# Optimization experiments

Hardware: AMD Instinct MI355X
Metric: run time of the kernel (lower is better)

Reference implementation:

```python
import jax, jax.numpy as jnp
import numpy as np


def setup_inputs() -> dict:
    key = jax.random.key(0)
    ks = jax.random.split(key, 4)
    B, S, D, H, E = 2, 2048, 1024, 4096, 8
    scale_in = 1.0 / np.sqrt(D)
    scale_h = 1.0 / np.sqrt(H)
    return {
        "x": jax.random.normal(ks[0], (B, S, D), dtype=jnp.float32),
        "Wr": jax.random.normal(ks[1], (E, D), dtype=jnp.float32) * scale_in,
        "br": jnp.zeros((E,), dtype=jnp.float32),
        "W1": jax.random.normal(ks[2], (E, H, D), dtype=jnp.float32) * scale_in,
        "b1": jnp.zeros((E, H), dtype=jnp.float32),
        "W2": jax.random.normal(ks[3], (E, D, H), dtype=jnp.float32) * scale_h,
        "b2": jnp.zeros((E, D), dtype=jnp.float32),
        "top_k": 2,
    }


def reference(x, Wr, br, W1, b1, W2, b2, top_k):
    B, S, D = x.shape
    E = Wr.shape[0]
    x_flat = x.reshape(-1, D)                                   # [N, D]
    # Router: top-k logits, softmax over the selected k values only
    logits = x_flat @ Wr.T + br                                 # [N, E]
    top_vals, top_idx = jax.lax.top_k(logits, top_k)            # [N, k]
    gates = jax.nn.softmax(top_vals, axis=-1)                   # [N, k]
    # Per-expert combine weight: gate_e[n, e] = sum_k gates[n, k] * 1[top_idx[n,k]==e]
    gate_e = jnp.einsum("nk,nke->ne", gates,
                        jax.nn.one_hot(top_idx, E, dtype=x.dtype))  # [N, E]
    # Dense all-expert MLP (grouped GEMM), then masked combine. Same math as
    # the per-expert gather/scatter loop: unselected experts get zero gate.
    h = jax.nn.relu(jnp.einsum("nd,ehd->neh", x_flat, W1) + b1)     # [N, E, H]
    y = jnp.einsum("neh,edh->ned", h, W2) + b2                      # [N, E, D]
    out = jnp.einsum("ned,ne->nd", y, gate_e)                       # [N, D]
    return out.reshape(B, S, D)
```

## Files before the change

kernel.cpp:

```cpp
#include <hip/hip_runtime.h>
#include <hip/hip_bf16.h>
#include <stdint.h>

#define N_TOK 4096
#define D_ 1024
#define H_ 4096
#define E_ 8
#define NSLOT (N_TOK*2)
#define BM 128
#define BN 128
#define BK 32
#define MAXT 72

typedef __attribute__((ext_vector_type(8))) short short8;
typedef __attribute__((ext_vector_type(4))) float floatx4;
typedef unsigned int u32;

__device__ __forceinline__ unsigned short f2bf(float f){
    union { float f; unsigned int u; } c; c.f = f;
    unsigned int u = c.u;
    unsigned int r = (u + 0x7fffu + ((u >> 16) & 1u)) >> 16;
    return (unsigned short)r;
}

__device__ __forceinline__ void async16(const void* g, void* l){
    __builtin_amdgcn_global_load_lds(
        (const __attribute__((address_space(1))) u32*)g,
        (__attribute__((address_space(3))) u32*)l, 16, 0, 0);
}


__global__ __launch_bounds__(256) void router_kernel(
    const float* __restrict__ x, const float* __restrict__ Wr,
    const float* __restrict__ br, int* __restrict__ topIdx,
    float* __restrict__ topGate)
{
    int n = blockIdx.x * 4 + (threadIdx.x >> 6);
    int lane = threadIdx.x & 63;
    const float4* xp = (const float4*)(x + (size_t)n * D_);
    float acc[E_];
#pragma unroll
    for (int e = 0; e < E_; e++) acc[e] = 0.f;
#pragma unroll
    for (int j = 0; j < 4; j++){
        int idx = j * 64 + lane;
        float4 xv = xp[idx];
#pragma unroll
        for (int e = 0; e < E_; e++){
            float4 wv = ((const float4*)(Wr + (size_t)e * D_))[idx];
            acc[e] += xv.x*wv.x + xv.y*wv.y + xv.z*wv.z + xv.w*wv.w;
        }
    }
#pragma unroll
    for (int e = 0; e < E_; e++){
        float v = acc[e];
        for (int off = 32; off > 0; off >>= 1) v += __shfl_xor(v, off, 64);
        acc[e] = v;
    }
    if (lane == 0){
        float best = -1e30f, second = -1e30f; int bi = 0, si = 0;
#pragma unroll
        for (int e = 0; e < E_; e++){
            float v = acc[e] + br[e];
            if (v > best){ second = best; si = bi; best = v; bi = e; }
            else if (v > second){ second = v; si = e; }
        }
        float e1 = __expf(second - best);
        float denom = 1.f + e1;
        topIdx[n*2+0] = bi;  topIdx[n*2+1] = si;
        topGate[n*2+0] = 1.f/denom;  topGate[n*2+1] = e1/denom;
    }
}

__global__ __launch_bounds__(256) void hist_kernel(
    const int* __restrict__ topIdx, int* __restrict__ hdr)
{
    __shared__ int c[E_];
    int t = threadIdx.x;
    if (t < E_) c[t] = 0;
    __syncthreads();
    int e = topIdx[blockIdx.x * 256 + t];
    atomicAdd(&c[e], 1);
    __syncthreads();
    if (t < E_) hdr[256 + blockIdx.x * E_ + t] = c[t];
}

__global__ __launch_bounds__(64) void scan2_kernel(int* __restrict__ hdr)
{
    __shared__ int cnt[32 * E_];
    __shared__ int tot[E_];
    __shared__ int offs[E_ + 1];
    int t = threadIdx.x;
    for (int i = t; i < 32 * E_; i += 64) cnt[i] = hdr[256 + i];
    __syncthreads();
    if (t < E_){
        int s = 0;
        for (int b = 0; b < 32; b++) s += cnt[b * E_ + t];
        tot[t] = s;
    }
    __syncthreads();
    if (t == 0){
        int o = 0;
        for (int e = 0; e < E_; e++){ offs[e] = o; o += tot[e]; }
        offs[E_] = o;
    }
    __syncthreads();
    if (t < E_ + 1) hdr[16 + t] = offs[t];
    if (t < E_){
        int run = offs[t];
        for (int b = 0; b < 32; b++){ hdr[512 + b * E_ + t] = run; run += cnt[b * E_ + t]; }
    }
    if (t == 0){
        int tn = 0;
        for (int e = 0; e < E_; e++){
            int nt = (tot[e] + BM - 1) >> 7;
            for (int i = 0; i < nt; i++){ hdr[32 + tn] = e; hdr[112 + tn] = offs[e] + (i << 7); tn++; }
        }
        for (; tn < MAXT; tn++){ hdr[32 + tn] = -1; hdr[112 + tn] = 0; }
    }
}

__global__ __launch_bounds__(256) void pos_kernel(
    const int* __restrict__ topIdx, const float* __restrict__ topGate,
    const int* __restrict__ hdr, int* __restrict__ posOf,
    int* __restrict__ rowTok, float* __restrict__ rowGate)
{
    __shared__ int c[E_];
    int t = threadIdx.x;
    if (t < E_) c[t] = 0;
    __syncthreads();
    int slot = blockIdx.x * 256 + t;
    int e = topIdx[slot];
    int r = atomicAdd(&c[e], 1);
    int pos = hdr[512 + blockIdx.x * E_ + e] + r;
    posOf[slot] = pos;
    rowTok[pos] = slot >> 1;
    rowGate[pos] = topGate[slot];
}

__global__ __launch_bounds__(256) void copy_kernel(
    const float* __restrict__ x, const int* __restrict__ posOf,
    unsigned short* __restrict__ xg)
{
    int slot = blockIdx.x * 4 + (threadIdx.x >> 6);
    int lane = threadIdx.x & 63;
    int n = slot >> 1;
    int pos = posOf[slot];
    const float4* xp = (const float4*)(x + (size_t)n * D_);
    ushort4* op = (ushort4*)(xg + (size_t)pos * D_);
#pragma unroll
    for (int j = 0; j < 4; j++){
        float4 v = xp[j * 64 + lane];
        ushort4 o; o.x=f2bf(v.x); o.y=f2bf(v.y); o.z=f2bf(v.z); o.w=f2bf(v.w);
        op[j * 64 + lane] = o;
    }
}

template<int MODE>
__global__ __launch_bounds__(256) void moe_gemm(
    const unsigned short* __restrict__ A, int Ktot,
    const float* __restrict__ Wbase, size_t wStride,
    const float* __restrict__ biasBase, int biasStride,
    const int* __restrict__ hdr,
    const int* __restrict__ rowTok, const float* __restrict__ rowGate,
    unsigned short* __restrict__ hout, float* __restrict__ out)
{
    const int bx = blockIdx.x, by = blockIdx.y;
    int e = hdr[32 + bx];
    if (e < 0) return;
    int rowBase = hdr[112 + bx];
    int validRows = hdr[16 + e + 1] - rowBase;

    __shared__ __align__(16) unsigned short As[BM * BK];
    __shared__ __align__(16) float Bs[BN * BK];

    const float* Wexp  = Wbase + (size_t)e * wStride + (size_t)(by * BN) * Ktot;
    const float* biasE = biasBase + (size_t)e * biasStride + by * BN;

    const int tid  = threadIdx.x;
    const int lane = tid & 63, wave = tid >> 6;
    const int wm = wave & 1, wn = wave >> 1;
    const int l16 = lane & 15, quad = lane >> 4;

    floatx4 acc[4][4];
#pragma unroll
    for (int mi = 0; mi < 4; mi++)
#pragma unroll
        for (int ni = 0; ni < 4; ni++)
            acc[mi][ni] = (floatx4){0.f,0.f,0.f,0.f};

    int aS[2], aRow[2], aCol[2];
#pragma unroll
    for (int i = 0; i < 2; i++){
        int s = wave * 128 + i * 64 + lane;
        aS[i] = s;
        int r = rowBase + (s >> 2);
        aRow[i] = r < (NSLOT - 1) ? r : (NSLOT - 1);
        aCol[i] = (s & 3) * 8;
    }
    int bS[4], bRow[4], bCol[4];
#pragma unroll
    for (int i = 0; i < 4; i++){
        int s = wave * 256 + i * 64 + lane;
        bS[i] = s;
        int r = s >> 3, c = s & 7;
        bRow[i] = r;
        bCol[i] = (c ^ (r & 7)) * 4;
    }

    for (int k0 = 0; k0 < Ktot; k0 += BK){
#pragma unroll
        for (int i = 0; i < 2; i++)
            async16(A + (size_t)aRow[i] * Ktot + k0 + aCol[i], (char*)As + aS[i] * 16);
#pragma unroll
        for (int i = 0; i < 4; i++)
            async16(Wexp + (size_t)bRow[i] * Ktot + k0 + bCol[i], (char*)Bs + bS[i] * 16);
        __syncthreads();

        short8 af[4];
#pragma unroll
        for (int mi = 0; mi < 4; mi++){
            int r = wm * 64 + mi * 16 + l16;
            af[mi] = *(const short8*)(As + r * BK + quad * 8);
        }
        short8 bfr[4];
#pragma unroll
        for (int ni = 0; ni < 4; ni++){
            int n = wn * 64 + ni * 16 + l16;
            int g0 = (2 * quad)     ^ (n & 7);
            int g1 = (2 * quad + 1) ^ (n & 7);
            float4 u0 = *(const float4*)(Bs + n * BK + g0 * 4);
            float4 u1 = *(const float4*)(Bs + n * BK + g1 * 4);
            union { short8 s; __hip_bfloat162 h[4]; } u;
            u.h[0] = __float22bfloat162_rn(make_float2(u0.x, u0.y));
            u.h[1] = __float22bfloat162_rn(make_float2(u0.z, u0.w));
            u.h[2] = __float22bfloat162_rn(make_float2(u1.x, u1.y));
            u.h[3] = __float22bfloat162_rn(make_float2(u1.z, u1.w));
            bfr[ni] = u.s;
        }
#pragma unroll
        for (int mi = 0; mi < 4; mi++)
#pragma unroll
            for (int ni = 0; ni < 4; ni++)
                acc[mi][ni] = __builtin_amdgcn_mfma_f32_16x16x32_bf16(
                    af[mi], bfr[ni], acc[mi][ni], 0, 0, 0);
        __syncthreads();
    }

#pragma unroll
    for (int mi = 0; mi < 4; mi++){
#pragma unroll
        for (int r = 0; r < 4; r++){
            int rl = wm * 64 + mi * 16 + quad * 4 + r;
            if (rl >= validRows) continue;
            int grow = rowBase + rl;
            int   tok  = 0;
            float gate = 0.f;
            if (MODE == 2){ tok = rowTok[grow]; gate = rowGate[grow]; }
#pragma unroll
            for (int ni = 0; ni < 4; ni++){
                int gcol = by * BN + wn * 64 + ni * 16 + l16;
                float v = acc[mi][ni][r] + biasE[wn * 64 + ni * 16 + l16];
                if (MODE == 1){
                    v = v > 0.f ? v : 0.f;
                    hout[(size_t)grow * H_ + gcol] = f2bf(v);
                } else {
                    atomicAdd(out + (size_t)tok * D_ + gcol, gate * v);
                }
            }
        }
    }
}

extern "C" void kernel_launch(void* const* d_in, const int* in_sizes, int n_in,
                              void* d_out, int out_size, void* d_ws, size_t ws_size,
                              hipStream_t stream)
{
    (void)in_sizes; (void)n_in; (void)ws_size;
    const float* x  = (const float*)d_in[0];
    const float* Wr = (const float*)d_in[1];
    const float* br = (const float*)d_in[2];
    const float* W1 = (const float*)d_in[3];
    const float* b1 = (const float*)d_in[4];
    const float* W2 = (const float*)d_in[5];
    const float* b2 = (const float*)d_in[6];
    float* out = (float*)d_out;

    char* ws = (char*)d_ws;
    int*   hdr     = (int*)ws;
    int*   topIdx  = (int*)  (ws + 4096);
    float* topGate = (float*)(ws + 36864);
    int*   posOf   = (int*)  (ws + 69632);
    int*   rowTok  = (int*)  (ws + 102400);
    float* rowGate = (float*)(ws + 135168);
    unsigned short* xg   = (unsigned short*)(ws + 262144);
    unsigned short* hbuf = (unsigned short*)(ws + 17039360);

    hipMemsetAsync(d_out, 0, (size_t)out_size * sizeof(float), stream);

    router_kernel<<<N_TOK/4, 256, 0, stream>>>(x, Wr, br, topIdx, topGate);
    hist_kernel<<<32, 256, 0, stream>>>(topIdx, hdr);
    scan2_kernel<<<1, 64, 0, stream>>>(hdr);
    pos_kernel<<<32, 256, 0, stream>>>(topIdx, topGate, hdr, posOf, rowTok, rowGate);
    copy_kernel<<<NSLOT/4, 256, 0, stream>>>(x, posOf, xg);
    moe_gemm<1><<<dim3(MAXT, H_/BN), 256, 0, stream>>>(
        xg, D_, W1, (size_t)H_ * D_, b1, H_, hdr, rowTok, rowGate, hbuf, nullptr);
    moe_gemm<2><<<dim3(MAXT, D_/BN), 256, 0, stream>>>(
        hbuf, H_, W2, (size_t)D_ * H_, b2, D_, hdr, rowTok, rowGate, nullptr, out);
}
```

Measured before the change: 649.0 us.

## Pre-convert expert weights to bf16, add split-K for second GEMM and grouped tile order

When the workspace is large enough, W1 and W2 are converted to bf16 in separate passes before the grouped GEMMs. The GEMMs then load bf16 tiles directly, which halves weight traffic and removes the per-tile fp32-to-bf16 conversion. The second GEMM is split along K into two z-slices that accumulate through atomics, with bias added only by slice zero. Block indices are also remapped so groups of eight column tiles run together for better L2 reuse. The conversion passes read 256MB and write 128MB on every call, and the split-K doubles the atomic traffic into the output.

```diff
diff --git a/kernel.cpp b/kernel.cpp
--- a/kernel.cpp
+++ b/kernel.cpp
@@ -29,6 +29,16 @@
         (__attribute__((address_space(3))) u32*)l, 16, 0, 0);
 }
 
+__global__ __launch_bounds__(256) void cvt_kernel(
+    const float* __restrict__ src, unsigned short* __restrict__ dst, int n4)
+{
+    int stride = gridDim.x * 256;
+    for (int i = blockIdx.x * 256 + threadIdx.x; i < n4; i += stride){
+        float4 v = ((const float4*)src)[i];
+        ushort4 o; o.x=f2bf(v.x); o.y=f2bf(v.y); o.z=f2bf(v.z); o.w=f2bf(v.w);
+        ((ushort4*)dst)[i] = o;
+    }
+}
 
 __global__ __launch_bounds__(256) void router_kernel(
     const float* __restrict__ x, const float* __restrict__ Wr,
@@ -156,25 +166,33 @@
     }
 }
 
-template<int MODE>
+template<int MODE, bool BF16B>
 __global__ __launch_bounds__(256) void moe_gemm(
     const unsigned short* __restrict__ A, int Ktot,
-    const float* __restrict__ Wbase, size_t wStride,
+    const void* __restrict__ Wbase, size_t wStride,
     const float* __restrict__ biasBase, int biasStride,
     const int* __restrict__ hdr,
     const int* __restrict__ rowTok, const float* __restrict__ rowGate,
     unsigned short* __restrict__ hout, float* __restrict__ out)
 {
-    const int bx = blockIdx.x, by = blockIdx.y;
+    int gid = blockIdx.y * gridDim.x + blockIdx.x;
+    int per = gridDim.x * 8;
+    int g = gid / per, rr = gid % per;
+    int by = g * 8 + (rr & 7);
+    int bx = rr >> 3;
+
     int e = hdr[32 + bx];
     if (e < 0) return;
     int rowBase = hdr[112 + bx];
     int validRows = hdr[16 + e + 1] - rowBase;
 
+    int kChunk = Ktot / gridDim.z;
+    int kStart = blockIdx.z * kChunk;
+
     __shared__ __align__(16) unsigned short As[BM * BK];
-    __shared__ __align__(16) float Bs[BN * BK];
-
-    const float* Wexp  = Wbase + (size_t)e * wStride + (size_t)(by * BN) * Ktot;
+    __shared__ __align__(16) unsigned short BsH[BF16B ? BN * BK : 1];
+    __shared__ __align__(16) float BsF[BF16B ? 1 : BN * BK];
+
     const float* biasE = biasBase + (size_t)e * biasStride + by * BN;
 
     const int tid  = threadIdx.x;
@@ -192,66 +210,96 @@
     int aS[2], aRow[2], aCol[2];
 #pragma unroll
     for (int i = 0; i < 2; i++){
-        int s = wave * 128 + i * 64 + lane;
+        int s = i * 256 + tid;
         aS[i] = s;
         int r = rowBase + (s >> 2);
         aRow[i] = r < (NSLOT - 1) ? r : (NSLOT - 1);
         aCol[i] = (s & 3) * 8;
     }
-    int bS[4], bRow[4], bCol[4];
-#pragma unroll
-    for (int i = 0; i < 4; i++){
-        int s = wave * 256 + i * 64 + lane;
-        bS[i] = s;
-        int r = s >> 3, c = s & 7;
-        bRow[i] = r;
-        bCol[i] = (c ^ (r & 7)) * 4;
-    }
-
-    for (int k0 = 0; k0 < Ktot; k0 += BK){
-#pragma unroll
-        for (int i = 0; i < 2; i++)
-            async16(A + (size_t)aRow[i] * Ktot + k0 + aCol[i], (char*)As + aS[i] * 16);
-#pragma unroll
-        for (int i = 0; i < 4; i++)
-            async16(Wexp + (size_t)bRow[i] * Ktot + k0 + bCol[i], (char*)Bs + bS[i] * 16);
-        __syncthreads();
-
-        short8 af[4];
-#pragma unroll
-        for (int mi = 0; mi < 4; mi++){
-            int r = wm * 64 + mi * 16 + l16;
-            af[mi] = *(const short8*)(As + r * BK + quad * 8);
-        }
-        short8 bfr[4];
-#pragma unroll
-        for (int ni = 0; ni < 4; ni++){
-            int n = wn * 64 + ni * 16 + l16;
-            int g0 = (2 * quad)     ^ (n & 7);
-            int g1 = (2 * quad + 1) ^ (n & 7);
-            float4 u0 = *(const float4*)(Bs + n * BK + g0 * 4);
-            float4 u1 = *(const float4*)(Bs + n * BK + g1 * 4);
-            union { short8 s; __hip_bfloat162 h[4]; } u;
-            u.h[0] = __float22bfloat162_rn(make_float2(u0.x, u0.y));
-            u.h[1] = __float22bfloat162_rn(make_float2(u0.z, u0.w));
-            u.h[2] = __float22bfloat162_rn(make_float2(u1.x, u1.y));
-            u.h[3] = __float22bfloat162_rn(make_float2(u1.z, u1.w));
-            bfr[ni] = u.s;
-        }
-#pragma unroll
-        for (int mi = 0; mi < 4; mi++)
+
+    if (BF16B){
+        const unsigned short* Wexp = (const unsigned short*)Wbase
+            + (size_t)e * wStride + (size_t)(by * BN) * Ktot;
+        for (int k0 = kStart; k0 < kStart + kChunk; k0 += BK){
+#pragma unroll
+            for (int i = 0; i < 2; i++)
+                async16(A + (size_t)aRow[i] * Ktot + k0 + aCol[i], (char*)As + aS[i] * 16);
+#pragma unroll
+            for (int i = 0; i < 2; i++){
+                int s = i * 256 + tid;
+                async16(Wexp + (size_t)(s >> 2) * Ktot + k0 + (s & 3) * 8,
+                        (char*)BsH + s * 16);
+            }
+            __syncthreads();
+            short8 af[4], bfr[4];
+#pragma unroll
+            for (int mi = 0; mi < 4; mi++)
+                af[mi] = *(const short8*)(As + (wm*64 + mi*16 + l16) * BK + quad * 8);
 #pragma unroll
             for (int ni = 0; ni < 4; ni++)
-                acc[mi][ni] = __builtin_amdgcn_mfma_f32_16x16x32_bf16(
-                    af[mi], bfr[ni], acc[mi][ni], 0, 0, 0);
-        __syncthreads();
-    }
-
+                bfr[ni] = *(const short8*)(BsH + (wn*64 + ni*16 + l16) * BK + quad * 8);
+#pragma unroll
+            for (int mi = 0; mi < 4; mi++)
+#pragma unroll
+                for (int ni = 0; ni < 4; ni++)
+                    acc[mi][ni] = __builtin_amdgcn_mfma_f32_16x16x32_bf16(
+                        af[mi], bfr[ni], acc[mi][ni], 0, 0, 0);
+            __syncthreads();
+        }
+    } else {
+        const float* Wexp = (const float*)Wbase
+            + (size_t)e * wStride + (size_t)(by * BN) * Ktot;
+        int bS[4], bRow[4], bCol[4];
+#pragma unroll
+        for (int i = 0; i < 4; i++){
+            int s = i * 256 + tid;
+            bS[i] = s;
+            int r = s >> 3, c = s & 7;
+            bRow[i] = r;
+            bCol[i] = (c ^ (r & 7)) * 4;
+        }
+        for (int k0 = kStart; k0 < kStart + kChunk; k0 += BK){
+#pragma unroll
+            for (int i = 0; i < 2; i++)
+                async16(A + (size_t)aRow[i] * Ktot + k0 + aCol[i], (char*)As + aS[i] * 16);
+#pragma unroll
+            for (int i = 0; i < 4; i++)
+                async16(Wexp + (size_t)bRow[i] * Ktot + k0 + bCol[i], (char*)BsF + bS[i] * 16);
+            __syncthreads();
+            short8 af[4], bfr[4];
+#pragma unroll
+            for (int mi = 0; mi < 4; mi++)
+                af[mi] = *(const short8*)(As + (wm*64 + mi*16 + l16) * BK + quad * 8);
+#pragma unroll
+            for (int ni = 0; ni < 4; ni++){
+                int n = wn*64 + ni*16 + l16;
+                int g0 = (2*quad)     ^ (n & 7);
+                int g1 = (2*quad + 1) ^ (n & 7);
+                float4 u0 = *(const float4*)(BsF + n * BK + g0 * 4);
+                float4 u1 = *(const float4*)(BsF + n * BK + g1 * 4);
+                union { short8 s; __hip_bfloat162 h[4]; } u;
+                u.h[0] = __float22bfloat162_rn(make_float2(u0.x, u0.y));
+                u.h[1] = __float22bfloat162_rn(make_float2(u0.z, u0.w));
+                u.h[2] = __float22bfloat162_rn(make_float2(u1.x, u1.y));
+                u.h[3] = __float22bfloat162_rn(make_float2(u1.z, u1.w));
+                bfr[ni] = u.s;
+            }
+#pragma unroll
+            for (int mi = 0; mi < 4; mi++)
+#pragma unroll
+                for (int ni = 0; ni < 4; ni++)
+                    acc[mi][ni] = __builtin_amdgcn_mfma_f32_16x16x32_bf16(
+                        af[mi], bfr[ni], acc[mi][ni], 0, 0, 0);
+            __syncthreads();
+        }
+    }
+
+    bool addB = (MODE == 1) || (blockIdx.z == 0);
 #pragma unroll
     for (int mi = 0; mi < 4; mi++){
 #pragma unroll
         for (int r = 0; r < 4; r++){
-            int rl = wm * 64 + mi * 16 + quad * 4 + r;
+            int rl = wm*64 + mi*16 + quad*4 + r;
             if (rl >= validRows) continue;
             int grow = rowBase + rl;
             int   tok  = 0;
@@ -259,8 +307,9 @@
             if (MODE == 2){ tok = rowTok[grow]; gate = rowGate[grow]; }
 #pragma unroll
             for (int ni = 0; ni < 4; ni++){
-                int gcol = by * BN + wn * 64 + ni * 16 + l16;
-                float v = acc[mi][ni][r] + biasE[wn * 64 + ni * 16 + l16];
+                int lcol = wn*64 + ni*16 + l16;
+                int gcol = by * BN + lcol;
+                float v = acc[mi][ni][r] + (addB ? biasE[lcol] : 0.f);
                 if (MODE == 1){
                     v = v > 0.f ? v : 0.f;
                     hout[(size_t)grow * H_ + gcol] = f2bf(v);
@@ -276,7 +325,7 @@
                               void* d_out, int out_size, void* d_ws, size_t ws_size,
                               hipStream_t stream)
 {
-    (void)in_sizes; (void)n_in; (void)ws_size;
+    (void)in_sizes; (void)n_in;
     const float* x  = (const float*)d_in[0];
     const float* Wr = (const float*)d_in[1];
     const float* br = (const float*)d_in[2];
@@ -295,6 +344,9 @@
     float* rowGate = (float*)(ws + 135168);
     unsigned short* xg   = (unsigned short*)(ws + 262144);
     unsigned short* hbuf = (unsigned short*)(ws + 17039360);
+    unsigned short* w1b  = (unsigned short*)(ws + 84148224);
+    unsigned short* w2b  = (unsigned short*)(ws + 151257088);
+    const bool full = ws_size >= 218365952ull;
 
     hipMemsetAsync(d_out, 0, (size_t)out_size * sizeof(float), stream);
 
@@ -303,8 +355,18 @@
     scan2_kernel<<<1, 64, 0, stream>>>(hdr);
     pos_kernel<<<32, 256, 0, stream>>>(topIdx, topGate, hdr, posOf, rowTok, rowGate);
     copy_kernel<<<NSLOT/4, 256, 0, stream>>>(x, posOf, xg);
-    moe_gemm<1><<<dim3(MAXT, H_/BN), 256, 0, stream>>>(
-        xg, D_, W1, (size_t)H_ * D_, b1, H_, hdr, rowTok, rowGate, hbuf, nullptr);
-    moe_gemm<2><<<dim3(MAXT, D_/BN), 256, 0, stream>>>(
-        hbuf, H_, W2, (size_t)D_ * H_, b2, D_, hdr, rowTok, rowGate, nullptr, out);
-}
+
+    if (full){
+        cvt_kernel<<<2048, 256, 0, stream>>>(W1, w1b, (E_*H_*D_)/4);
+        cvt_kernel<<<2048, 256, 0, stream>>>(W2, w2b, (E_*D_*H_)/4);
+        moe_gemm<1,true><<<dim3(MAXT, H_/BN, 1), 256, 0, stream>>>(
+            xg, D_, w1b, (size_t)H_ * D_, b1, H_, hdr, rowTok, rowGate, hbuf, nullptr);
+        moe_gemm<2,true><<<dim3(MAXT, D_/BN, 2), 256, 0, stream>>>(
+            hbuf, H_, w2b, (size_t)D_ * H_, b2, D_, hdr, rowTok, rowGate, nullptr, out);
+    } else {
+        moe_gemm<1,false><<<dim3(MAXT, H_/BN, 1), 256, 0, stream>>>(
+            xg, D_, W1, (size_t)H_ * D_, b1, H_, hdr, rowTok, rowGate, hbuf, nullptr);
+        moe_gemm<2,false><<<dim3(MAXT, D_/BN, 2), 256, 0, stream>>>(
+            hbuf, H_, W2, (size_t)D_ * H_, b2, D_, hdr, rowTok, rowGate, nullptr, out);
+    }
+}
```

Result: slower. 664.4 us (+2.4%).
